# Kernel optimization log

Hardware: AMD Instinct MI355X
Metric: run time of the kernel (lower is better)

The kernel has to match this reference:

```python
import jax, jax.numpy as jnp
import numpy as np

NUM_BANDS = 30
SPLIT_FREQ = 30
M_PARAM = 1
DIM = 2048
BATCH = 16384


def _dct_mat(N):
    # Orthonormal DCT-II matrix D: dct(x) = x @ D.T, idct(y) = y @ D
    n = np.arange(N, dtype=np.float64)
    kk = n[:, None]
    M = np.cos(np.pi * (n + 0.5) * kk / N)
    s = np.full(N, np.sqrt(2.0 / N))
    s[0] = np.sqrt(1.0 / N)
    return jnp.asarray((M * s[:, None]).astype(np.float32))


def _band_scale(freq_weights, k, N):
    # Precompute the per-frequency scale vector the torch loop applies band-by-band.
    pts = np.linspace(0, N - 1, NUM_BANDS + 1).astype(np.int64)  # torch .long() truncation
    scale = jnp.ones((N,), dtype=freq_weights.dtype)
    for i in range(NUM_BANDS):
        s, e = int(pts[i]), int(pts[i + 1])
        if e <= SPLIT_FREQ:
            f = 1.0 + freq_weights[i] * k * (1.0 - i / NUM_BANDS)
        else:
            f = 1.0 - freq_weights[i] * k * (1.0 - (i - NUM_BANDS // M_PARAM) / NUM_BANDS)
        scale = scale.at[s:e].set(f)  # bands are disjoint; base is 1
    return scale


def setup_inputs() -> dict:
    key = jax.random.key(0)
    ks = jax.random.split(key, 6)
    g = 0.02  # small init like xavier_uniform with gain 0.5
    return {
        "x": jax.random.normal(ks[0], (BATCH, DIM), dtype=jnp.float32),
        "freq_weights": jnp.ones((NUM_BANDS,), dtype=jnp.float32),
        "k": jnp.float32(0.3),
        "W1": jax.random.normal(ks[1], (1024, DIM), dtype=jnp.float32) * g,
        "b1": jnp.zeros((1024,), dtype=jnp.float32),
        "W2": jax.random.normal(ks[2], (512, 1024), dtype=jnp.float32) * g,
        "b2": jnp.zeros((512,), dtype=jnp.float32),
        "Wmu": jax.random.normal(ks[3], (256, 512), dtype=jnp.float32) * g,
        "bmu": jnp.zeros((256,), dtype=jnp.float32),
        "Wlv": jax.random.normal(ks[4], (256, 512), dtype=jnp.float32) * g,
        "blv": jnp.zeros((256,), dtype=jnp.float32),
    }


def reference(x, freq_weights, k, W1, b1, W2, b2, Wmu, bmu, Wlv, blv):
    N = x.shape[-1]
    D = _dct_mat(N)
    # DCT -> per-band reweight -> IDCT, fused as two matmuls and one vector multiply
    xd = (x @ D.T) * _band_scale(freq_weights, k, N)
    xe = xd @ D
    h = jax.nn.relu(xe @ W1.T + b1)
    h = jax.nn.relu(h @ W2.T + b2)
    mu = h @ Wmu.T + bmu
    logvar = h @ Wlv.T + blv
    return (mu, logvar)
```

## Files before the change

kernel.cpp:

```cpp
#include <hip/hip_runtime.h>
#include <hip/hip_bf16.h>
#include <math.h>

#define DIM 2048
#define BATCH 16384

typedef __attribute__((ext_vector_type(8))) short short8;
typedef __attribute__((ext_vector_type(4))) float floatx4;
typedef unsigned short ushort_t;

__device__ __forceinline__ ushort_t f2bf(float f) {
    union { float f; unsigned u; } v; v.f = f;
    unsigned r = v.u + 0x7FFFu + ((v.u >> 16) & 1u);
    return (ushort_t)(r >> 16);
}

__global__ void k_scale(const float* __restrict__ fw, const float* __restrict__ kp,
                        float* __restrict__ s) {
    int n = blockIdx.x * blockDim.x + threadIdx.x;
    if (n >= DIM) return;
    float kv = kp[0];
    float f = 1.0f;
    for (int i = 0; i < 30; ++i) {
        long s0 = (long)((double)i       * (double)(DIM - 1) / 30.0);
        long e0 = (long)((double)(i + 1) * (double)(DIM - 1) / 30.0);
        if (n >= s0 && n < e0) {
            if (e0 <= 30)
                f = 1.0f + fw[i] * kv * (1.0f - (float)i / 30.0f);
            else
                f = 1.0f - fw[i] * kv * (1.0f - (float)(i - 30) / 30.0f);
        }
    }
    s[n] = f;
}

__global__ void k_gen_d(ushort_t* __restrict__ D, ushort_t* __restrict__ Dt) {
    int idx = blockIdx.x * blockDim.x + threadIdx.x;
    int r = idx >> 11;
    int c = idx & (DIM - 1);
    const float w  = 7.6699039394282058e-4f;
    const float s0 = 0.02209708691207961f;
    const float s1 = 0.03125f;
    int m1 = ((2 * c + 1) * r) & (4 * DIM - 1);
    int m2 = ((2 * r + 1) * c) & (4 * DIM - 1);
    float v1 = cosf(w * (float)m1) * (r == 0 ? s0 : s1);
    float v2 = cosf(w * (float)m2) * (c == 0 ? s0 : s1);
    D[idx]  = f2bf(v1);
    Dt[idx] = f2bf(v2);
}

#define U_X   4194304
#define U_W1   262144
#define U_W2    65536
#define U_WH    16384
__global__ void k_cast_all(const float* __restrict__ X,  const float* __restrict__ W1,
                           const float* __restrict__ W2, const float* __restrict__ Wmu,
                           const float* __restrict__ Wlv,
                           ushort_t* __restrict__ Xbf, ushort_t* __restrict__ W1bf,
                           ushort_t* __restrict__ W2bf, ushort_t* __restrict__ Wcat) {
    int i = blockIdx.x * blockDim.x + threadIdx.x;
    const float* src; ushort_t* dst; int u;
    if (i < U_X)                          { src = X;   dst = Xbf;                u = i; }
    else if (i < U_X + U_W1)              { src = W1;  dst = W1bf;               u = i - U_X; }
    else if (i < U_X + U_W1 + U_W2)       { src = W2;  dst = W2bf;               u = i - U_X - U_W1; }
    else if (i < U_X + U_W1 + U_W2 + U_WH){ src = Wmu; dst = Wcat;               u = i - U_X - U_W1 - U_W2; }
    else                                  { src = Wlv; dst = Wcat + 8 * U_WH;    u = i - U_X - U_W1 - U_W2 - U_WH; }
    const float4* p = reinterpret_cast<const float4*>(src) + 2 * (size_t)u;
    float4 a = p[0], b = p[1];
    short8 r;
    r[0] = (short)f2bf(a.x); r[1] = (short)f2bf(a.y);
    r[2] = (short)f2bf(a.z); r[3] = (short)f2bf(a.w);
    r[4] = (short)f2bf(b.x); r[5] = (short)f2bf(b.y);
    r[6] = (short)f2bf(b.z); r[7] = (short)f2bf(b.w);
    *reinterpret_cast<short8*>(dst + 8 * (size_t)u) = r;
}

template<int TM, int TN, int EPI>
__global__ __launch_bounds__(256)
void gemm_bt(const ushort_t* __restrict__ A, const ushort_t* __restrict__ B,
             ushort_t* __restrict__ Cb, float* __restrict__ Cf,
             const float* __restrict__ ep0, const float* __restrict__ ep1,
             int M, int N, int K) {
    constexpr int BM = 32 * TM;
    constexpr int BN = 32 * TN;
    __shared__ __align__(16) ushort_t As[BM * 32];
    __shared__ __align__(16) ushort_t Bs[BN * 32];

    const int tid  = threadIdx.x;
    const int lane = tid & 63;
    const int wave = tid >> 6;
    const int wm   = wave >> 1;
    const int wn   = wave & 1;
    const int q    = lane >> 4;
    const int l16  = lane & 15;

    const int tilesM = M / BM;
    const int tilesN = N / BN;
    const int bid = (int)blockIdx.x;
    const int xcd = bid & 7;
    const int j   = bid >> 3;
    const int bm  = xcd * (tilesM >> 3) + j / tilesN;
    const int bn  = j % tilesN;

    floatx4 acc[TM][TN];
    #pragma unroll
    for (int i = 0; i < TM; ++i)
        #pragma unroll
        for (int jj = 0; jj < TN; ++jj)
            acc[i][jj] = (floatx4){0.f, 0.f, 0.f, 0.f};

    const long aBase = (long)bm * BM * K;
    const long bBase = (long)bn * BN * K;

    for (int kt = 0; kt < K; kt += 32) {
        __syncthreads();
        #pragma unroll
        for (int i = 0; i < BM / 64; ++i) {
            int idx = tid + i * 256;
            int row = idx >> 2, seg = idx & 3;
            int gseg = seg ^ ((row >> 1) & 3);
            const ushort_t* g = A + aBase + (long)row * K + kt + gseg * 8;
            __builtin_amdgcn_global_load_lds(
                (const __attribute__((address_space(1))) void*)g,
                (__attribute__((address_space(3))) void*)(As + idx * 8),
                16, 0, 0);
        }
        #pragma unroll
        for (int i = 0; i < BN / 64; ++i) {
            int idx = tid + i * 256;
            int row = idx >> 2, seg = idx & 3;
            int gseg = seg ^ ((row >> 1) & 3);
            const ushort_t* g = B + bBase + (long)row * K + kt + gseg * 8;
            __builtin_amdgcn_global_load_lds(
                (const __attribute__((address_space(1))) void*)g,
                (__attribute__((address_space(3))) void*)(Bs + idx * 8),
                16, 0, 0);
        }
        __syncthreads();

        short8 af[TM], bfr[TN];
        #pragma unroll
        for (int t = 0; t < TM; ++t) {
            int srow = wm * TM * 16 + t * 16 + l16;
            int rseg = q ^ ((srow >> 1) & 3);
            af[t] = *reinterpret_cast<const short8*>(&As[srow * 32 + rseg * 8]);
        }
        #pragma unroll
        for (int t = 0; t < TN; ++t) {
            int srow = wn * TN * 16 + t * 16 + l16;
            int rseg = q ^ ((srow >> 1) & 3);
            bfr[t] = *reinterpret_cast<const short8*>(&Bs[srow * 32 + rseg * 8]);
        }
        #pragma unroll
        for (int i = 0; i < TM; ++i)
            #pragma unroll
            for (int jj = 0; jj < TN; ++jj)
                acc[i][jj] = __builtin_amdgcn_mfma_f32_16x16x32_bf16(
                    af[i], bfr[jj], acc[i][jj], 0, 0, 0);
    }

    #pragma unroll
    for (int i = 0; i < TM; ++i) {
        #pragma unroll
        for (int jj = 0; jj < TN; ++jj) {
            #pragma unroll
            for (int r = 0; r < 4; ++r) {
                int row = bm * BM + wm * TM * 16 + i * 16 + q * 4 + r;
                int col = bn * BN + wn * TN * 16 + jj * 16 + l16;
                float v = acc[i][jj][r];
                if constexpr (EPI == 0) {
                    Cb[(long)row * N + col] = f2bf(v * ep0[col]);
                } else if constexpr (EPI == 1) {
                    Cb[(long)row * N + col] = f2bf(v);
                } else if constexpr (EPI == 2) {
                    v += ep0[col];
                    v = v > 0.f ? v : 0.f;
                    Cb[(long)row * N + col] = f2bf(v);
                } else {
                    const int half = N >> 1;
                    if (col < half)
                        Cf[(long)row * half + col] = v + ep0[col];
                    else
                        Cf[(long)M * half + (long)row * half + (col - half)] = v + ep1[col - half];
                }
            }
        }
    }
}

extern "C" void kernel_launch(void* const* d_in, const int* in_sizes, int n_in,
                              void* d_out, int out_size, void* d_ws, size_t ws_size,
                              hipStream_t stream) {
    const float* x   = (const float*)d_in[0];
    const float* fw  = (const float*)d_in[1];
    const float* kp  = (const float*)d_in[2];
    const float* W1  = (const float*)d_in[3];
    const float* b1  = (const float*)d_in[4];
    const float* W2  = (const float*)d_in[5];
    const float* b2  = (const float*)d_in[6];
    const float* Wmu = (const float*)d_in[7];
    const float* bmu = (const float*)d_in[8];
    const float* Wlv = (const float*)d_in[9];
    const float* blv = (const float*)d_in[10];
    float* out = (float*)d_out;

    char* ws = (char*)d_ws;
    const size_t MB = 1024 * 1024;
    ushort_t* W1bf = (ushort_t*)(ws + 0);
    ushort_t* Dbf  = (ushort_t*)(ws + 4  * MB);
    ushort_t* Dtbf = (ushort_t*)(ws + 12 * MB);
    ushort_t* T1sT = (ushort_t*)(ws + 20 * MB);
    ushort_t* H1   = (ushort_t*)(ws + 0);
    ushort_t* H2   = (ushort_t*)(ws + 32 * MB);
    ushort_t* M1T  = (ushort_t*)(ws + 48 * MB);
    ushort_t* W2bf = (ushort_t*)(ws + 52 * MB);
    ushort_t* Wcat = (ushort_t*)(ws + 53 * MB);
    float*    svec = (float*)   (ws + 54 * MB);
    ushort_t* Xbf  = (ushort_t*)(ws + 55 * MB);

    hipLaunchKernelGGL(k_scale, dim3(DIM / 256), dim3(256), 0, stream, fw, kp, svec);
    hipLaunchKernelGGL(k_gen_d, dim3(DIM * DIM / 256), dim3(256), 0, stream, Dbf, Dtbf);

    hipLaunchKernelGGL(k_cast_all, dim3((U_X + U_W1 + U_W2 + 2 * U_WH) / 256), dim3(256), 0, stream,
                       x, W1, W2, Wmu, Wlv, Xbf, W1bf, W2bf, Wcat);

    hipLaunchKernelGGL((gemm_bt<2, 2, 0>), dim3((1024 / 64) * (2048 / 64)), dim3(256), 0, stream,
                       W1bf, Dbf, T1sT, nullptr, svec, nullptr, 1024, 2048, 2048);
    hipLaunchKernelGGL((gemm_bt<2, 2, 1>), dim3((1024 / 64) * (2048 / 64)), dim3(256), 0, stream,
                       T1sT, Dtbf, M1T, nullptr, nullptr, nullptr, 1024, 2048, 2048);
    hipLaunchKernelGGL((gemm_bt<4, 4, 2>), dim3((BATCH / 128) * (1024 / 128)), dim3(256), 0, stream,
                       Xbf, M1T, H1, nullptr, b1, nullptr, BATCH, 1024, 2048);
    hipLaunchKernelGGL((gemm_bt<4, 4, 2>), dim3((BATCH / 128) * (512 / 128)), dim3(256), 0, stream,
                       H1, W2bf, H2, nullptr, b2, nullptr, BATCH, 512, 1024);
    hipLaunchKernelGGL((gemm_bt<4, 4, 3>), dim3((BATCH / 128) * (512 / 128)), dim3(256), 0, stream,
                       H2, Wcat, nullptr, out, bmu, blv, BATCH, 512, 512);

    (void)in_sizes; (void)n_in; (void)out_size; (void)ws_size;
}
```

Baseline: 434.8 us.

## Fuse fp32-to-bf16 cast of x into the first batch GEMM's A-tile load

Removes the separate pass that cast the 16384x2048 fp32 input to bf16 in workspace. The x@M1 GEMM now loads fp32 A tiles into registers, prefetching the next k-slice during the MFMAs, then converts and writes them to LDS with the same swizzle. This saves a write and a re-read of a 64MB bf16 copy, at the cost of reading twice the bytes per A tile inside the GEMM, more registers, and a register-staged load in place of direct global-to-LDS loads.

```diff
diff --git a/kernel.cpp b/kernel.cpp
--- a/kernel.cpp
+++ b/kernel.cpp
@@ -8,11 +8,18 @@
 typedef __attribute__((ext_vector_type(8))) short short8;
 typedef __attribute__((ext_vector_type(4))) float floatx4;
 typedef unsigned short ushort_t;
+typedef unsigned int uint_t;
 
 __device__ __forceinline__ ushort_t f2bf(float f) {
     union { float f; unsigned u; } v; v.f = f;
     unsigned r = v.u + 0x7FFFu + ((v.u >> 16) & 1u);
     return (ushort_t)(r >> 16);
+}
+
+__device__ __forceinline__ uint_t cvt2bf(float a, float b) {
+    __hip_bfloat162 h = __float22bfloat162_rn(float2{a, b});
+    union { __hip_bfloat162 h; uint_t u; } v; v.h = h;
+    return v.u;
 }
 
 __global__ void k_scale(const float* __restrict__ fw, const float* __restrict__ kp,
@@ -49,22 +56,19 @@
     Dt[idx] = f2bf(v2);
 }
 
-#define U_X   4194304
 #define U_W1   262144
 #define U_W2    65536
 #define U_WH    16384
-__global__ void k_cast_all(const float* __restrict__ X,  const float* __restrict__ W1,
-                           const float* __restrict__ W2, const float* __restrict__ Wmu,
-                           const float* __restrict__ Wlv,
-                           ushort_t* __restrict__ Xbf, ushort_t* __restrict__ W1bf,
-                           ushort_t* __restrict__ W2bf, ushort_t* __restrict__ Wcat) {
+__global__ void k_cast_w(const float* __restrict__ W1, const float* __restrict__ W2,
+                         const float* __restrict__ Wmu, const float* __restrict__ Wlv,
+                         ushort_t* __restrict__ W1bf, ushort_t* __restrict__ W2bf,
+                         ushort_t* __restrict__ Wcat) {
     int i = blockIdx.x * blockDim.x + threadIdx.x;
     const float* src; ushort_t* dst; int u;
-    if (i < U_X)                          { src = X;   dst = Xbf;                u = i; }
-    else if (i < U_X + U_W1)              { src = W1;  dst = W1bf;               u = i - U_X; }
-    else if (i < U_X + U_W1 + U_W2)       { src = W2;  dst = W2bf;               u = i - U_X - U_W1; }
-    else if (i < U_X + U_W1 + U_W2 + U_WH){ src = Wmu; dst = Wcat;               u = i - U_X - U_W1 - U_W2; }
-    else                                  { src = Wlv; dst = Wcat + 8 * U_WH;    u = i - U_X - U_W1 - U_W2 - U_WH; }
+    if (i < U_W1)                    { src = W1;  dst = W1bf;             u = i; }
+    else if (i < U_W1 + U_W2)        { src = W2;  dst = W2bf;             u = i - U_W1; }
+    else if (i < U_W1 + U_W2 + U_WH) { src = Wmu; dst = Wcat;             u = i - U_W1 - U_W2; }
+    else                             { src = Wlv; dst = Wcat + 8 * U_WH;  u = i - U_W1 - U_W2 - U_WH; }
     const float4* p = reinterpret_cast<const float4*>(src) + 2 * (size_t)u;
     float4 a = p[0], b = p[1];
     short8 r;
@@ -75,12 +79,13 @@
     *reinterpret_cast<short8*>(dst + 8 * (size_t)u) = r;
 }
 
-template<int TM, int TN, int EPI>
-__global__ __launch_bounds__(256)
-void gemm_bt(const ushort_t* __restrict__ A, const ushort_t* __restrict__ B,
-             ushort_t* __restrict__ Cb, float* __restrict__ Cf,
-             const float* __restrict__ ep0, const float* __restrict__ ep1,
-             int M, int N, int K) {
+template<int TM, int TN, int EPI, bool AF32>
+__device__ __forceinline__ void gemm_core(
+        const ushort_t* __restrict__ A, const float* __restrict__ Af,
+        const ushort_t* __restrict__ B,
+        ushort_t* __restrict__ Cb, float* __restrict__ Cf,
+        const float* __restrict__ ep0, const float* __restrict__ ep1,
+        int M, int N, int K) {
     constexpr int BM = 32 * TM;
     constexpr int BN = 32 * TN;
     __shared__ __align__(16) ushort_t As[BM * 32];
@@ -112,18 +117,40 @@
     const long aBase = (long)bm * BM * K;
     const long bBase = (long)bn * BN * K;
 
+    float4 pf[4];
+    const float* abase = nullptr;
+    if constexpr (AF32) {
+        abase = Af + aBase + (long)(tid >> 3) * K + (tid & 7) * 4;
+        #pragma unroll
+        for (int i = 0; i < 4; ++i)
+            pf[i] = *reinterpret_cast<const float4*>(abase + (long)i * 32 * K);
+    }
+
     for (int kt = 0; kt < K; kt += 32) {
         __syncthreads();
-        #pragma unroll
-        for (int i = 0; i < BM / 64; ++i) {
-            int idx = tid + i * 256;
-            int row = idx >> 2, seg = idx & 3;
-            int gseg = seg ^ ((row >> 1) & 3);
-            const ushort_t* g = A + aBase + (long)row * K + kt + gseg * 8;
-            __builtin_amdgcn_global_load_lds(
-                (const __attribute__((address_space(1))) void*)g,
-                (__attribute__((address_space(3))) void*)(As + idx * 8),
-                16, 0, 0);
+        if constexpr (AF32) {
+            const int rowb = tid >> 3, fseg = tid & 7;
+            #pragma unroll
+            for (int i = 0; i < 4; ++i) {
+                int row  = rowb + i * 32;
+                int lseg = (fseg >> 1) ^ ((row >> 1) & 3);
+                uint2 w;
+                w.x = cvt2bf(pf[i].x, pf[i].y);
+                w.y = cvt2bf(pf[i].z, pf[i].w);
+                *reinterpret_cast<uint2*>(As + row * 32 + lseg * 8 + (fseg & 1) * 4) = w;
+            }
+        } else {
+            #pragma unroll
+            for (int i = 0; i < BM / 64; ++i) {
+                int idx = tid + i * 256;
+                int row = idx >> 2, seg = idx & 3;
+                int gseg = seg ^ ((row >> 1) & 3);
+                const ushort_t* g = A + aBase + (long)row * K + kt + gseg * 8;
+                __builtin_amdgcn_global_load_lds(
+                    (const __attribute__((address_space(1))) void*)g,
+                    (__attribute__((address_space(3))) void*)(As + idx * 8),
+                    16, 0, 0);
+            }
         }
         #pragma unroll
         for (int i = 0; i < BN / 64; ++i) {
@@ -150,6 +177,14 @@
             int srow = wn * TN * 16 + t * 16 + l16;
             int rseg = q ^ ((srow >> 1) & 3);
             bfr[t] = *reinterpret_cast<const short8*>(&Bs[srow * 32 + rseg * 8]);
+        }
+        if constexpr (AF32) {
+            if (kt + 32 < K) {
+                const float* ab = abase + kt + 32;
+                #pragma unroll
+                for (int i = 0; i < 4; ++i)
+                    pf[i] = *reinterpret_cast<const float4*>(ab + (long)i * 32 * K);
+            }
         }
         #pragma unroll
         for (int i = 0; i < TM; ++i)
@@ -188,6 +223,27 @@
     }
 }
 
+__global__ __launch_bounds__(256) void g0_w1d(const ushort_t* A, const ushort_t* B,
+        ushort_t* Cb, const float* ep0, int M, int N, int K) {
+    gemm_core<2, 2, 0, false>(A, nullptr, B, Cb, nullptr, ep0, nullptr, M, N, K);
+}
+__global__ __launch_bounds__(256) void g1_m1(const ushort_t* A, const ushort_t* B,
+        ushort_t* Cb, int M, int N, int K) {
+    gemm_core<2, 2, 1, false>(A, nullptr, B, Cb, nullptr, nullptr, nullptr, M, N, K);
+}
+__global__ __launch_bounds__(256) void g2_xm1(const float* Af, const ushort_t* B,
+        ushort_t* Cb, const float* ep0, int M, int N, int K) {
+    gemm_core<4, 4, 2, true>(nullptr, Af, B, Cb, nullptr, ep0, nullptr, M, N, K);
+}
+__global__ __launch_bounds__(256) void g3_h2(const ushort_t* A, const ushort_t* B,
+        ushort_t* Cb, const float* ep0, int M, int N, int K) {
+    gemm_core<4, 4, 2, false>(A, nullptr, B, Cb, nullptr, ep0, nullptr, M, N, K);
+}
+__global__ __launch_bounds__(256) void g4_head(const ushort_t* A, const ushort_t* B,
+        float* Cf, const float* ep0, const float* ep1, int M, int N, int K) {
+    gemm_core<4, 4, 3, false>(A, nullptr, B, nullptr, Cf, ep0, ep1, M, N, K);
+}
+
 extern "C" void kernel_launch(void* const* d_in, const int* in_sizes, int n_in,
                               void* d_out, int out_size, void* d_ws, size_t ws_size,
                               hipStream_t stream) {
@@ -216,24 +272,22 @@
     ushort_t* W2bf = (ushort_t*)(ws + 52 * MB);
     ushort_t* Wcat = (ushort_t*)(ws + 53 * MB);
     float*    svec = (float*)   (ws + 54 * MB);
-    ushort_t* Xbf  = (ushort_t*)(ws + 55 * MB);
 
     hipLaunchKernelGGL(k_scale, dim3(DIM / 256), dim3(256), 0, stream, fw, kp, svec);
     hipLaunchKernelGGL(k_gen_d, dim3(DIM * DIM / 256), dim3(256), 0, stream, Dbf, Dtbf);
-
-    hipLaunchKernelGGL(k_cast_all, dim3((U_X + U_W1 + U_W2 + 2 * U_WH) / 256), dim3(256), 0, stream,
-                       x, W1, W2, Wmu, Wlv, Xbf, W1bf, W2bf, Wcat);
-
-    hipLaunchKernelGGL((gemm_bt<2, 2, 0>), dim3((1024 / 64) * (2048 / 64)), dim3(256), 0, stream,
-                       W1bf, Dbf, T1sT, nullptr, svec, nullptr, 1024, 2048, 2048);
-    hipLaunchKernelGGL((gemm_bt<2, 2, 1>), dim3((1024 / 64) * (2048 / 64)), dim3(256), 0, stream,
-                       T1sT, Dtbf, M1T, nullptr, nullptr, nullptr, 1024, 2048, 2048);
-    hipLaunchKernelGGL((gemm_bt<4, 4, 2>), dim3((BATCH / 128) * (1024 / 128)), dim3(256), 0, stream,
-                       Xbf, M1T, H1, nullptr, b1, nullptr, BATCH, 1024, 2048);
-    hipLaunchKernelGGL((gemm_bt<4, 4, 2>), dim3((BATCH / 128) * (512 / 128)), dim3(256), 0, stream,
-                       H1, W2bf, H2, nullptr, b2, nullptr, BATCH, 512, 1024);
-    hipLaunchKernelGGL((gemm_bt<4, 4, 3>), dim3((BATCH / 128) * (512 / 128)), dim3(256), 0, stream,
-                       H2, Wcat, nullptr, out, bmu, blv, BATCH, 512, 512);
+    hipLaunchKernelGGL(k_cast_w, dim3((U_W1 + U_W2 + 2 * U_WH) / 256), dim3(256), 0, stream,
+                       W1, W2, Wmu, Wlv, W1bf, W2bf, Wcat);
+
+    hipLaunchKernelGGL(g0_w1d, dim3((1024 / 64) * (2048 / 64)), dim3(256), 0, stream,
+                       W1bf, Dbf, T1sT, svec, 1024, 2048, 2048);
+    hipLaunchKernelGGL(g1_m1, dim3((1024 / 64) * (2048 / 64)), dim3(256), 0, stream,
+                       T1sT, Dtbf, M1T, 1024, 2048, 2048);
+    hipLaunchKernelGGL(g2_xm1, dim3((BATCH / 128) * (1024 / 128)), dim3(256), 0, stream,
+                       x, M1T, H1, b1, BATCH, 1024, 2048);
+    hipLaunchKernelGGL(g3_h2, dim3((BATCH / 128) * (512 / 128)), dim3(256), 0, stream,
+                       H1, W2bf, H2, b2, BATCH, 512, 1024);
+    hipLaunchKernelGGL(g4_head, dim3((BATCH / 128) * (512 / 128)), dim3(256), 0, stream,
+                       H2, Wcat, out, bmu, blv, BATCH, 512, 512);
 
     (void)in_sizes; (void)n_in; (void)out_size; (void)ws_size;
 }
```

Result: slower. 455.2 us (+4.7%).
